# Kernel tuning notes

Measured on AMD Instinct MI355X. Metric: run time of the kernel, lower is better.

The kernel has to match this reference:

```python
import jax, jax.numpy as jnp
import numpy as np

D_MODEL = 1024
N_HEADS = 16
D_FF = 4096
B, T = 4, 2048
EPS = 1e-5


def layernorm(x, g, b):
    mu = jnp.mean(x, axis=-1, keepdims=True)
    var = jnp.var(x, axis=-1, keepdims=True)
    return (x - mu) * jax.lax.rsqrt(var + EPS) * g + b


def setup_inputs() -> dict:
    key = jax.random.key(0)
    ks = jax.random.split(key, 8)
    s = 0.02
    return {
        "x": jax.random.normal(ks[0], (B, T, D_MODEL), jnp.float32),
        "ln1_g": jnp.ones((D_MODEL,), jnp.float32),
        "ln1_b": jnp.zeros((D_MODEL,), jnp.float32),
        "wq": jax.random.normal(ks[1], (D_MODEL, D_MODEL), jnp.float32) * s,
        "bq": jnp.zeros((D_MODEL,), jnp.float32),
        "wk": jax.random.normal(ks[2], (D_MODEL, D_MODEL), jnp.float32) * s,
        "bk": jnp.zeros((D_MODEL,), jnp.float32),
        "wv": jax.random.normal(ks[3], (D_MODEL, D_MODEL), jnp.float32) * s,
        "bv": jnp.zeros((D_MODEL,), jnp.float32),
        "wo": jax.random.normal(ks[4], (D_MODEL, D_MODEL), jnp.float32) * s,
        "bo": jnp.zeros((D_MODEL,), jnp.float32),
        "ln2_g": jnp.ones((D_MODEL,), jnp.float32),
        "ln2_b": jnp.zeros((D_MODEL,), jnp.float32),
        "w1": jax.random.normal(ks[5], (D_FF, D_MODEL), jnp.float32) * s,
        "b1": jnp.zeros((D_FF,), jnp.float32),
        "w2": jax.random.normal(ks[6], (D_MODEL, D_FF), jnp.float32) * s,
        "b2": jnp.zeros((D_MODEL,), jnp.float32),
    }


def reference(x, ln1_g, ln1_b, wq, bq, wk, bk, wv, bv, wo, bo,
              ln2_g, ln2_b, w1, b1, w2, b2):
    d_k = D_MODEL // N_HEADS
    # --- attention sublayer (pre-LN) ---
    h = layernorm(x, ln1_g, ln1_b)                       # [B,T,D]
    q = (h @ wq.T + bq).reshape(B, T, N_HEADS, d_k)
    k = (h @ wk.T + bk).reshape(B, T, N_HEADS, d_k)
    v = (h @ wv.T + bv).reshape(B, T, N_HEADS, d_k)
    scores = jnp.einsum("bqhd,bkhd->bhqk", q, k) / jnp.sqrt(jnp.float32(d_k))
    attn = jax.nn.softmax(scores, axis=-1)               # [B,H,T,T]
    o = jnp.einsum("bhqk,bkhd->bqhd", attn, v).reshape(B, T, D_MODEL)
    x = x + (o @ wo.T + bo)
    # --- FFN sublayer ---
    h2 = layernorm(x, ln2_g, ln2_b)
    h2 = jax.nn.gelu(h2 @ w1.T + b1, approximate=False)  # torch GELU = exact erf
    x = x + (h2 @ w2.T + b2)
    return x
```

## Files before the change

kernel.cpp:

```cpp
#include <hip/hip_runtime.h>
#include <math.h>


#define D_MODEL 1024
#define D_FF    4096
#define NH      16
#define BATCH   4
#define SEQ     2048
#define DK      64
#define MTOK    (BATCH*SEQ)
#define NBH     (BATCH*NH)

typedef __bf16 bf16;
typedef _Float16 f16;
typedef bf16  bf16x4 __attribute__((ext_vector_type(4)));
typedef bf16  bf16x8 __attribute__((ext_vector_type(8)));
typedef f16   f16x4  __attribute__((ext_vector_type(4)));
typedef f16   f16x8  __attribute__((ext_vector_type(8)));
typedef __fp16 hf16x2 __attribute__((ext_vector_type(2)));
typedef __fp16 hf16x4 __attribute__((ext_vector_type(4)));
typedef __fp16 hf16x8 __attribute__((ext_vector_type(8)));
typedef float f32x4  __attribute__((ext_vector_type(4)));

__device__ __forceinline__ void gload_lds16(const void* g, void* l) {
  __builtin_amdgcn_global_load_lds(
      (__attribute__((address_space(1))) void*)g,
      (__attribute__((address_space(3))) void*)l, 16, 0, 0);
}

#define BAR() __builtin_amdgcn_s_barrier()
#define WAIT_VM0() do { asm volatile("s_waitcnt vmcnt(0)" ::: "memory"); \
  __builtin_amdgcn_sched_barrier(0); } while (0)

__device__ __forceinline__ float gelu_fast(float x) {
  float ax = fabsf(x) * 0.70710678118654752f;
  float t  = 1.0f / (1.0f + 0.3275911f * ax);
  float p  = t * (0.254829592f + t * (-0.284496736f + t * (1.421413741f +
             t * (-1.453152027f + t * 1.061405429f))));
  float e  = __builtin_amdgcn_exp2f(ax * ax * -1.4426950408889634f);
  float er = 1.0f - p * e;
  er = __builtin_copysignf(er, x);
  return 0.5f * x * (1.0f + er);
}

__global__ __launch_bounds__(256) void cast_w(const float* __restrict__ s,
                                              bf16* __restrict__ d, int n) {
  int i = (blockIdx.x * 256 + threadIdx.x) * 4;
  if (i >= n) return;
  float4 v = *(const float4*)(s + i);
  bf16x4 o;
  o[0] = (bf16)v.x; o[1] = (bf16)v.y; o[2] = (bf16)v.z; o[3] = (bf16)v.w;
  *(bf16x4*)(d + i) = o;
}

__global__ __launch_bounds__(256) void ln_kernel(const float* __restrict__ x,
                                                 const float* __restrict__ g,
                                                 const float* __restrict__ b,
                                                 bf16* __restrict__ out) {
  int row = blockIdx.x;
  int tid = threadIdx.x;
  const float* xr = x + (size_t)row * D_MODEL;
  float4 v = *(const float4*)(xr + tid * 4);
  float s  = v.x + v.y + v.z + v.w;
  float sq = v.x*v.x + v.y*v.y + v.z*v.z + v.w*v.w;
  #pragma unroll
  for (int off = 1; off < 64; off <<= 1) {
    s  += __shfl_xor(s,  off, 64);
    sq += __shfl_xor(sq, off, 64);
  }
  __shared__ float ls[4], lq[4];
  int wid = tid >> 6, lane = tid & 63;
  if (lane == 0) { ls[wid] = s; lq[wid] = sq; }
  __syncthreads();
  s  = ls[0] + ls[1] + ls[2] + ls[3];
  sq = lq[0] + lq[1] + lq[2] + lq[3];
  float mu   = s * (1.0f / D_MODEL);
  float var  = sq * (1.0f / D_MODEL) - mu * mu;
  float rstd = rsqrtf(var + 1e-5f);
  float4 gv = *(const float4*)(g + tid * 4);
  float4 bv = *(const float4*)(b + tid * 4);
  bf16x4 o;
  o[0] = (bf16)((v.x - mu) * rstd * gv.x + bv.x);
  o[1] = (bf16)((v.y - mu) * rstd * gv.y + bv.y);
  o[2] = (bf16)((v.z - mu) * rstd * gv.z + bv.z);
  o[3] = (bf16)((v.w - mu) * rstd * gv.w + bv.w);
  *(bf16x4*)(out + (size_t)row * D_MODEL + tid * 4) = o;
}

enum { EP_QKV = 0, EP_RESID = 1, EP_GELU = 2 };

#define QSCALE 0.18033688011112042f

template <int EP, int CFG>
__global__ __launch_bounds__(512) void gemm8p(
    const bf16* __restrict__ A, const bf16* __restrict__ W,
    const float* __restrict__ bias,
    const float* __restrict__ resid,
    float* __restrict__ out_f32,
    bf16* __restrict__ out_bf,
    int M, int N, int K) {
  constexpr int BM  = CFG ? 128 : 256;
  constexpr int BK  = CFG ? 64 : 32;
  constexpr int WM  = CFG ? 64 : 128;
  constexpr int FRN = WM / 16;
  constexpr int KKN = BK / 32;
  constexpr int RB  = BK * 2;
  constexpr int GR  = RB / 16;
  constexpr int RSH = CFG ? 7 : 6;
  constexpr int AB  = 16384;
  constexpr int TB  = AB + 256 * BK * 2;
  constexpr int L   = TB / 8192;

  __shared__ char lds[3 * TB];

  int tiles_n = N >> 8;
  int nwg = (M / BM) * tiles_n;
  int bid = blockIdx.x;
  int swz = (bid & 7) * (nwg >> 3) + (bid >> 3);
  int bm = swz / tiles_n, bn = swz % tiles_n;
  int m0 = bm * BM, n0 = bn << 8;
  int tid = threadIdx.x, wid = tid >> 6, lane = tid & 63;
  int wm = wid >> 2, wn = wid & 3;
  int l15 = lane & 15, l4 = lane >> 4;

  f32x4 acc[FRN][4];
  #pragma unroll
  for (int i = 0; i < FRN; i++)
    #pragma unroll
    for (int j = 0; j < 4; j++)
      #pragma unroll
      for (int e = 0; e < 4; e++) acc[i][j][e] = 0.f;

  auto STAGE = [&](int kt, int nb) {
    char* buf = lds + nb * TB;
    #pragma unroll
    for (int l = 0; l < L; ++l) {
      bool isA = l < 2;
      int o = (isA ? l : l - 2) * 8192 + tid * 16;
      int row = o >> RSH;
      int g = (o >> 4) & (GR - 1);
      int gs = g ^ (CFG ? (row & 7) : ((row >> 1) & 3));
      const bf16* src = (isA ? A + (size_t)(m0 + row) * K
                             : W + (size_t)(n0 + row) * K) + kt * BK + gs * 8;
      gload_lds16(src, buf + (isA ? 0 : AB) + o);
    }
  };

  int nt = K / BK;
  STAGE(0, 0);
  STAGE(1, 1);
  if constexpr (CFG) { asm volatile("s_waitcnt vmcnt(6)" ::: "memory"); }
  else               { asm volatile("s_waitcnt vmcnt(4)" ::: "memory"); }
  __builtin_amdgcn_sched_barrier(0);
  BAR();

  for (int t = 0; t < nt; ++t) {
    int cb = t % 3, nb = cb >= 1 ? cb - 1 : 2;
    const char* bc = lds + cb * TB;

    if (t + 2 < nt) STAGE(t + 2, nb);

    bf16x8 af[FRN][KKN], bfr[4][KKN];
    #pragma unroll
    for (int f = 0; f < FRN; ++f)
      #pragma unroll
      for (int kk = 0; kk < KKN; ++kk) {
        int row = wm * WM + f * 16 + l15;
        int g = (kk * 4 + l4) ^ (CFG ? (row & 7) : ((row >> 1) & 3));
        af[f][kk] = *(const bf16x8*)(bc + row * RB + g * 16);
      }
    #pragma unroll
    for (int fc = 0; fc < 4; ++fc)
      #pragma unroll
      for (int kk = 0; kk < KKN; ++kk) {
        int row = wn * 64 + fc * 16 + l15;
        int g = (kk * 4 + l4) ^ (CFG ? (row & 7) : ((row >> 1) & 3));
        bfr[fc][kk] = *(const bf16x8*)(bc + AB + row * RB + g * 16);
      }

    __builtin_amdgcn_s_setprio(1);
    #pragma unroll
    for (int f = 0; f < FRN; ++f)
      #pragma unroll
      for (int fc = 0; fc < 4; ++fc)
        #pragma unroll
        for (int kk = 0; kk < KKN; ++kk) {
          if (EP == EP_QKV)
            acc[f][fc] = __builtin_amdgcn_mfma_f32_16x16x32_bf16(af[f][kk], bfr[fc][kk],
                                                                 acc[f][fc], 0, 0, 0);
          else
            acc[f][fc] = __builtin_amdgcn_mfma_f32_16x16x32_bf16(bfr[fc][kk], af[f][kk],
                                                                 acc[f][fc], 0, 0, 0);
        }
    __builtin_amdgcn_s_setprio(0);

    if (t + 2 < nt) {
      if constexpr (CFG) { asm volatile("s_waitcnt vmcnt(6)" ::: "memory"); }
      else               { asm volatile("s_waitcnt vmcnt(4)" ::: "memory"); }
      __builtin_amdgcn_sched_barrier(0);
    } else if (t + 1 < nt) {
      WAIT_VM0();
    }
    BAR();
  }

  if (EP == EP_QKV) {
    #pragma unroll
    for (int i = 0; i < FRN; i++)
      #pragma unroll
      for (int j = 0; j < 4; j++) {
        int gm0 = m0 + wm * WM + i * 16 + (l4 << 2);
        int gn  = n0 + wn * 64 + j * 16 + l15;
        int which = gn >> 10;
        int nn = gn & 1023, head = nn >> 6, d = nn & 63;
        int bb = gm0 >> 11, t = gm0 & 2047;
        float bv = bias[gn];
        if (which == 2) {
          int sbase = (t & ~31) + ((t >> 2) & 3) * 8 + ((t >> 4) & 1) * 4;
          f16x4 pk;
          #pragma unroll
          for (int jj = 0; jj < 4; jj++) pk[jj] = (f16)(acc[i][j][jj] + bv);
          *(f16x4*)((f16*)out_bf + (size_t)2 * NBH * SEQ * DK +
                    ((size_t)(bb * NH + head) * DK + d) * SEQ + sbase) = pk;
        } else {
          float scale = (which == 0) ? QSCALE : 1.0f;
          #pragma unroll
          for (int jj = 0; jj < 4; jj++) {
            float cv = (acc[i][j][jj] + bv) * scale;
            size_t idx = (size_t)which * (NBH * SEQ * DK) +
                         ((size_t)(bb * NH + head) * SEQ + (t + jj)) * DK + d;
            out_bf[idx] = (bf16)cv;
          }
        }
      }
  } else {
    #pragma unroll
    for (int i = 0; i < FRN; i++) {
      int gm = m0 + wm * WM + i * 16 + l15;
      #pragma unroll
      for (int j = 0; j < 4; j++) {
        int gn = n0 + wn * 64 + j * 16 + (l4 << 2);
        float4 bv4 = *(const float4*)(bias + gn);
        size_t idx = (size_t)gm * N + gn;
        if (EP == EP_RESID) {
          float4 rv = *(const float4*)(resid + idx);
          float4 ov;
          ov.x = rv.x + acc[i][j][0] + bv4.x;
          ov.y = rv.y + acc[i][j][1] + bv4.y;
          ov.z = rv.z + acc[i][j][2] + bv4.z;
          ov.w = rv.w + acc[i][j][3] + bv4.w;
          *(float4*)(out_f32 + idx) = ov;
        } else {
          bf16x4 pk;
          pk[0] = (bf16)gelu_fast(acc[i][j][0] + bv4.x);
          pk[1] = (bf16)gelu_fast(acc[i][j][1] + bv4.y);
          pk[2] = (bf16)gelu_fast(acc[i][j][2] + bv4.z);
          pk[3] = (bf16)gelu_fast(acc[i][j][3] + bv4.w);
          *(bf16x4*)(out_bf + idx) = pk;
        }
      }
    }
  }
}

__global__ __launch_bounds__(512) void attn_kernel(
    const bf16* __restrict__ q, const bf16* __restrict__ k,
    const f16* __restrict__ vt, bf16* __restrict__ o) {
  __shared__ bf16 kt_lds[2][64 * 64];
  __shared__ f16  vt_lds[2][64 * 64];
  int bid = blockIdx.x;
  int swzb = (bid & 7) * 64 + (bid >> 3);
  int bh = swzb >> 3;
  int qt = swzb & 7;
  int t0 = qt << 8;
  int tid = threadIdx.x, wid = tid >> 6, lane = tid & 63;
  int l15 = lane & 15, l4 = lane >> 4;

  int kb0 = l15 * 128 + ((l4 ^ (l15 & 7)) << 4);
  int kb1 = l15 * 128 + (((4 + l4) ^ (l15 & 7)) << 4);
  int vb32[2];
  #pragma unroll
  for (int n = 0; n < 2; n++)
    vb32[n] = l15 * 128 + (((n * 4 + l4) ^ (l15 & 7)) << 4);

  bf16x8 qf[2][2];
  #pragma unroll
  for (int qr = 0; qr < 2; qr++) {
    const bf16* qbase = q + ((size_t)bh * SEQ + t0 + wid * 32 + qr * 16 + l15) * DK;
    qf[qr][0] = *(const bf16x8*)(qbase + (l4 << 3));
    qf[qr][1] = *(const bf16x8*)(qbase + 32 + (l4 << 3));
  }

  f16x8 vones8;
  #pragma unroll
  for (int e = 0; e < 8; e++) vones8[e] = (f16)1.f;
  float m_run[2] = {-1e30f, -1e30f};
  f32x4 acc_o[2][4];
  f32x4 acc_l[2];
  #pragma unroll
  for (int qr = 0; qr < 2; qr++) {
    #pragma unroll
    for (int nd = 0; nd < 4; nd++)
      #pragma unroll
      for (int e = 0; e < 4; e++) acc_o[qr][nd][e] = 0.f;
    #pragma unroll
    for (int e = 0; e < 4; e++) acc_l[qr][e] = 0.f;
  }

  int oK = tid * 16;
  int rowk = oK >> 7, gk = (oK >> 4) & 7;
  const bf16* gKsrc = k + ((size_t)bh * SEQ + rowk) * DK + ((gk ^ (rowk & 7)) << 3);
  int dV = oK >> 7, gd = (oK >> 4) & 7;
  const f16* gVsrc = vt + ((size_t)bh * DK + dV) * SEQ + ((gd ^ (dV & 7)) << 3);

  auto stage = [&](int buf, int t) {
    int kv0 = t * 64;
    gload_lds16(gKsrc + (size_t)kv0 * DK, (char*)&kt_lds[buf][0] + tid * 16);
    gload_lds16(gVsrc + kv0, (char*)&vt_lds[buf][0] + tid * 16);
  };

  stage(0, 0);
  WAIT_VM0();
  BAR();

  for (int t = 0; t < SEQ / 64; ++t) {
    int cur = t & 1;
    if (t < SEQ / 64 - 1) stage(cur ^ 1, t + 1);
    const char* kbase = (const char*)&kt_lds[cur][0];
    const char* vbase = (const char*)&vt_lds[cur][0];

    f32x4 accs[2][4];
    #pragma unroll
    for (int qr = 0; qr < 2; qr++)
      #pragma unroll
      for (int n = 0; n < 4; n++)
        #pragma unroll
        for (int e = 0; e < 4; e++) accs[qr][n][e] = 0.f;
    __builtin_amdgcn_s_setprio(1);
    #pragma unroll
    for (int n = 0; n < 4; n++) {
      bf16x8 kf0 = *(const bf16x8*)(kbase + kb0 + n * 2048);
      bf16x8 kf1 = *(const bf16x8*)(kbase + kb1 + n * 2048);
      #pragma unroll
      for (int qr = 0; qr < 2; qr++) {
        accs[qr][n] = __builtin_amdgcn_mfma_f32_16x16x32_bf16(kf0, qf[qr][0], accs[qr][n], 0, 0, 0);
        accs[qr][n] = __builtin_amdgcn_mfma_f32_16x16x32_bf16(kf1, qf[qr][1], accs[qr][n], 0, 0, 0);
      }
    }
    __builtin_amdgcn_s_setprio(0);

    f16x8 pa32[2][2];
    #pragma unroll
    for (int qr = 0; qr < 2; qr++) {
      float mloc = -1e30f;
      #pragma unroll
      for (int n = 0; n < 4; n++) {
        float a0 = fmaxf(accs[qr][n][0], accs[qr][n][1]);
        float a1 = fmaxf(accs[qr][n][2], accs[qr][n][3]);
        mloc = fmaxf(mloc, fmaxf(a0, a1));
      }
      float mt = fmaxf(mloc, __shfl_xor(mloc, 16, 64));
      mt = fmaxf(mt, __shfl_xor(mt, 32, 64));
      if (__any(mt > m_run[qr] + 8.0f)) {
        float mn = fmaxf(m_run[qr], mt);
        float sc = __builtin_amdgcn_exp2f(m_run[qr] - mn);
        m_run[qr] = mn;
        float scr0 = __shfl(sc, l4 * 20 + 0, 64);
        float scr1 = __shfl(sc, l4 * 20 + 1, 64);
        float scr2 = __shfl(sc, l4 * 20 + 2, 64);
        float scr3 = __shfl(sc, l4 * 20 + 3, 64);
        #pragma unroll
        for (int nd = 0; nd < 4; nd++) {
          acc_o[qr][nd][0] *= scr0; acc_o[qr][nd][1] *= scr1;
          acc_o[qr][nd][2] *= scr2; acc_o[qr][nd][3] *= scr3;
        }
        acc_l[qr][0] *= scr0; acc_l[qr][1] *= scr1;
        acc_l[qr][2] *= scr2; acc_l[qr][3] *= scr3;
      }
      #pragma unroll
      for (int n = 0; n < 2; n++) {
        float e0 = __builtin_amdgcn_exp2f(accs[qr][2*n][0] - m_run[qr]);
        float e1 = __builtin_amdgcn_exp2f(accs[qr][2*n][1] - m_run[qr]);
        float e2 = __builtin_amdgcn_exp2f(accs[qr][2*n][2] - m_run[qr]);
        float e3 = __builtin_amdgcn_exp2f(accs[qr][2*n][3] - m_run[qr]);
        float e4 = __builtin_amdgcn_exp2f(accs[qr][2*n+1][0] - m_run[qr]);
        float e5 = __builtin_amdgcn_exp2f(accs[qr][2*n+1][1] - m_run[qr]);
        float e6 = __builtin_amdgcn_exp2f(accs[qr][2*n+1][2] - m_run[qr]);
        float e7 = __builtin_amdgcn_exp2f(accs[qr][2*n+1][3] - m_run[qr]);
        hf16x2 p01 = __builtin_amdgcn_cvt_pkrtz(e0, e1);
        hf16x2 p23 = __builtin_amdgcn_cvt_pkrtz(e2, e3);
        hf16x2 p45 = __builtin_amdgcn_cvt_pkrtz(e4, e5);
        hf16x2 p67 = __builtin_amdgcn_cvt_pkrtz(e6, e7);
        hf16x4 lo = __builtin_shufflevector(p01, p23, 0, 1, 2, 3);
        hf16x4 hi = __builtin_shufflevector(p45, p67, 0, 1, 2, 3);
        hf16x8 cmb = __builtin_shufflevector(lo, hi, 0, 1, 2, 3, 4, 5, 6, 7);
        pa32[qr][n] = __builtin_bit_cast(f16x8, cmb);
      }
    }

    __builtin_amdgcn_s_setprio(1);
    #pragma unroll
    for (int n = 0; n < 2; n++) {
      #pragma unroll
      for (int nd = 0; nd < 4; nd++) {
        f16x8 vf = *(const f16x8*)(vbase + vb32[n] + nd * 2048);
        #pragma unroll
        for (int qr = 0; qr < 2; qr++)
          acc_o[qr][nd] = __builtin_amdgcn_mfma_f32_16x16x32_f16(pa32[qr][n], vf, acc_o[qr][nd], 0, 0, 0);
      }
      #pragma unroll
      for (int qr = 0; qr < 2; qr++)
        acc_l[qr] = __builtin_amdgcn_mfma_f32_16x16x32_f16(pa32[qr][n], vones8, acc_l[qr], 0, 0, 0);
    }
    __builtin_amdgcn_s_setprio(0);

    if (t < SEQ / 64 - 1) { WAIT_VM0(); }
    BAR();
  }

  int bb = bh >> 4, hh = bh & 15;
  #pragma unroll
  for (int qr = 0; qr < 2; qr++) {
    float rl0 = 1.0f / acc_l[qr][0], rl1 = 1.0f / acc_l[qr][1];
    float rl2 = 1.0f / acc_l[qr][2], rl3 = 1.0f / acc_l[qr][3];
    int rowb = t0 + wid * 32 + qr * 16 + l4 * 4;
    #pragma unroll
    for (int nd = 0; nd < 4; nd++) {
      int d = nd * 16 + l15;
      o[((size_t)bb * SEQ + rowb + 0) * D_MODEL + hh * DK + d] = (bf16)(acc_o[qr][nd][0] * rl0);
      o[((size_t)bb * SEQ + rowb + 1) * D_MODEL + hh * DK + d] = (bf16)(acc_o[qr][nd][1] * rl1);
      o[((size_t)bb * SEQ + rowb + 2) * D_MODEL + hh * DK + d] = (bf16)(acc_o[qr][nd][2] * rl2);
      o[((size_t)bb * SEQ + rowb + 3) * D_MODEL + hh * DK + d] = (bf16)(acc_o[qr][nd][3] * rl3);
    }
  }
}

extern "C" void kernel_launch(void* const* d_in, const int* in_sizes, int n_in,
                              void* d_out, int out_size, void* d_ws, size_t ws_size,
                              hipStream_t stream) {
  const float* x    = (const float*)d_in[0];
  const float* ln1g = (const float*)d_in[1];
  const float* ln1b = (const float*)d_in[2];
  const float* wq   = (const float*)d_in[3];
  const float* bq   = (const float*)d_in[4];
  const float* wk   = (const float*)d_in[5];
  const float* bk   = (const float*)d_in[6];
  const float* wv   = (const float*)d_in[7];
  const float* bv   = (const float*)d_in[8];
  const float* wo   = (const float*)d_in[9];
  const float* bo   = (const float*)d_in[10];
  const float* ln2g = (const float*)d_in[11];
  const float* ln2b = (const float*)d_in[12];
  const float* w1   = (const float*)d_in[13];
  const float* b1   = (const float*)d_in[14];
  const float* w2   = (const float*)d_in[15];
  const float* b2   = (const float*)d_in[16];
  float* out = (float*)d_out;

  char* ws = (char*)d_ws;
  bf16* wqkv_b = (bf16*)(ws);
  bf16* wo_b   = (bf16*)(ws + ((size_t)6  << 20));
  bf16* w1_b   = (bf16*)(ws + ((size_t)8  << 20));
  bf16* w2_b   = (bf16*)(ws + ((size_t)16 << 20));
  bf16* h_b    = (bf16*)(ws + ((size_t)24 << 20));
  bf16* qkv_b  = (bf16*)(ws + ((size_t)40 << 20));
  bf16* o_b    = (bf16*)(ws + ((size_t)88 << 20));
  bf16* ffn1_b = (bf16*)(ws + ((size_t)40 << 20));
  float* bqkv  = (float*)(ws + ((size_t)104 << 20));

  cast_w<<<1024, 256, 0, stream>>>(wq, wqkv_b, 1 << 20);
  cast_w<<<1024, 256, 0, stream>>>(wk, wqkv_b + (1 << 20), 1 << 20);
  cast_w<<<1024, 256, 0, stream>>>(wv, wqkv_b + (2 << 20), 1 << 20);
  cast_w<<<1024, 256, 0, stream>>>(wo, wo_b, 1 << 20);
  cast_w<<<4096, 256, 0, stream>>>(w1, w1_b, 1 << 22);
  cast_w<<<4096, 256, 0, stream>>>(w2, w2_b, 1 << 22);
  (void)hipMemcpyAsync(bqkv,        bq, 4096, hipMemcpyDeviceToDevice, stream);
  (void)hipMemcpyAsync(bqkv + 1024, bk, 4096, hipMemcpyDeviceToDevice, stream);
  (void)hipMemcpyAsync(bqkv + 2048, bv, 4096, hipMemcpyDeviceToDevice, stream);

  ln_kernel<<<MTOK, 256, 0, stream>>>(x, ln1g, ln1b, h_b);
  gemm8p<EP_QKV, 1><<<768, 512, 0, stream>>>(h_b, wqkv_b, bqkv, nullptr, nullptr,
                                             qkv_b, MTOK, 3072, 1024);
  attn_kernel<<<512, 512, 0, stream>>>(qkv_b, qkv_b + (size_t)NBH * SEQ * DK,
                                       (const f16*)(qkv_b + (size_t)2 * NBH * SEQ * DK),
                                       o_b);
  gemm8p<EP_RESID, 1><<<256, 512, 0, stream>>>(o_b, wo_b, bo, x, out, nullptr,
                                               MTOK, 1024, 1024);
  ln_kernel<<<MTOK, 256, 0, stream>>>(out, ln2g, ln2b, h_b);
  gemm8p<EP_GELU, 0><<<512, 512, 0, stream>>>(h_b, w1_b, b1, nullptr, nullptr,
                                              ffn1_b, MTOK, 4096, 1024);
  gemm8p<EP_RESID, 1><<<256, 512, 0, stream>>>(ffn1_b, w2_b, b2, out, out, nullptr,
                                               MTOK, 1024, 4096);
}
```

Baseline: 408.5 us.

## Use 256x256 GEMM tiles with quarter-staged double buffering for QKV and FFN1

Adds a new gemm256 kernel with 256x256 output tiles and BK=64, double-buffered in 128KB of LDS. Each k-step is split into four phases, one per B column fragment, and the next tile's loads are issued in quarter chunks between those phases. The QKV projection moves from 128x256 to 256x256 tiles, and FFN1 moves from BK=32 to 64, to raise data reuse per tile. The residual GEMMs get their own specialized kernel that keeps the old 128x256 configuration. In exchange there are many extra barriers per k-step, a large LDS footprint that limits occupancy, and fewer workgroups for QKV (384).

```diff
diff --git a/kernel.cpp b/kernel.cpp
--- a/kernel.cpp
+++ b/kernel.cpp
@@ -29,7 +29,11 @@
 }
 
 #define BAR() __builtin_amdgcn_s_barrier()
+#define LGKM0() do { asm volatile("s_waitcnt lgkmcnt(0)" ::: "memory"); \
+  __builtin_amdgcn_sched_barrier(0); } while (0)
 #define WAIT_VM0() do { asm volatile("s_waitcnt vmcnt(0)" ::: "memory"); \
+  __builtin_amdgcn_sched_barrier(0); } while (0)
+#define WAIT_VM4() do { asm volatile("s_waitcnt vmcnt(4)" ::: "memory"); \
   __builtin_amdgcn_sched_barrier(0); } while (0)
 
 __device__ __forceinline__ float gelu_fast(float x) {
@@ -88,128 +92,145 @@
 }
 
 enum { EP_QKV = 0, EP_RESID = 1, EP_GELU = 2 };
-
 #define QSCALE 0.18033688011112042f
 
-template <int EP, int CFG>
-__global__ __launch_bounds__(512) void gemm8p(
+template <int EP>
+__global__ __launch_bounds__(512, 2) void gemm256(
     const bf16* __restrict__ A, const bf16* __restrict__ W,
     const float* __restrict__ bias,
-    const float* __restrict__ resid,
-    float* __restrict__ out_f32,
     bf16* __restrict__ out_bf,
     int M, int N, int K) {
-  constexpr int BM  = CFG ? 128 : 256;
-  constexpr int BK  = CFG ? 64 : 32;
-  constexpr int WM  = CFG ? 64 : 128;
-  constexpr int FRN = WM / 16;
-  constexpr int KKN = BK / 32;
-  constexpr int RB  = BK * 2;
-  constexpr int GR  = RB / 16;
-  constexpr int RSH = CFG ? 7 : 6;
-  constexpr int AB  = 16384;
-  constexpr int TB  = AB + 256 * BK * 2;
-  constexpr int L   = TB / 8192;
-
-  __shared__ char lds[3 * TB];
-
+  __shared__ char lds[131072];
   int tiles_n = N >> 8;
-  int nwg = (M / BM) * tiles_n;
+  int nwg = (M >> 8) * tiles_n;
   int bid = blockIdx.x;
   int swz = (bid & 7) * (nwg >> 3) + (bid >> 3);
   int bm = swz / tiles_n, bn = swz % tiles_n;
-  int m0 = bm * BM, n0 = bn << 8;
+  int m0 = bm << 8, n0 = bn << 8;
   int tid = threadIdx.x, wid = tid >> 6, lane = tid & 63;
   int wm = wid >> 2, wn = wid & 3;
   int l15 = lane & 15, l4 = lane >> 4;
 
-  f32x4 acc[FRN][4];
-  #pragma unroll
-  for (int i = 0; i < FRN; i++)
-    #pragma unroll
-    for (int j = 0; j < 4; j++)
-      #pragma unroll
-      for (int e = 0; e < 4; e++) acc[i][j][e] = 0.f;
-
-  auto STAGE = [&](int kt, int nb) {
-    char* buf = lds + nb * TB;
-    #pragma unroll
-    for (int l = 0; l < L; ++l) {
-      bool isA = l < 2;
-      int o = (isA ? l : l - 2) * 8192 + tid * 16;
-      int row = o >> RSH;
-      int g = (o >> 4) & (GR - 1);
-      int gs = g ^ (CFG ? (row & 7) : ((row >> 1) & 3));
-      const bf16* src = (isA ? A + (size_t)(m0 + row) * K
-                             : W + (size_t)(n0 + row) * K) + kt * BK + gs * 8;
-      gload_lds16(src, buf + (isA ? 0 : AB) + o);
+  f32x4 acc[8][4];
+  #pragma unroll
+  for (int f = 0; f < 8; f++)
+    #pragma unroll
+    for (int n = 0; n < 4; n++)
+      #pragma unroll
+      for (int e = 0; e < 4; e++) acc[f][n][e] = 0.f;
+
+  auto STAGEH = [&](int h, int kt, int bsel) {
+    char* buf = lds + bsel * 65536;
+    #pragma unroll
+    for (int l = 0; l < 2; ++l) {
+      int o = h * 16384 + l * 8192 + tid * 16;
+      int row = (o >> 7) & 255;
+      int g = (o >> 4) & 7;
+      int gs = g ^ (row & 7);
+      const bf16* src = (h < 2 ? A + (size_t)(m0 + row) * K
+                               : W + (size_t)(n0 + row) * K) + kt * 64 + gs * 8;
+      gload_lds16(src, buf + o);
     }
   };
-
-  int nt = K / BK;
-  STAGE(0, 0);
-  STAGE(1, 1);
-  if constexpr (CFG) { asm volatile("s_waitcnt vmcnt(6)" ::: "memory"); }
-  else               { asm volatile("s_waitcnt vmcnt(4)" ::: "memory"); }
-  __builtin_amdgcn_sched_barrier(0);
+  auto RDB = [&](const char* bc, int n, int kk) -> bf16x8 {
+    int row = wn * 64 + n * 16 + l15;
+    return *(const bf16x8*)(bc + 32768 + row * 128 + (((kk << 2) + l4) ^ (row & 7)) * 16);
+  };
+
+  int nt = K >> 6;
+  STAGEH(0, 0, 0); STAGEH(1, 0, 0); STAGEH(2, 0, 0); STAGEH(3, 0, 0);
+  STAGEH(0, 1, 1); STAGEH(1, 1, 1);
+  WAIT_VM4();
   BAR();
 
   for (int t = 0; t < nt; ++t) {
-    int cb = t % 3, nb = cb >= 1 ? cb - 1 : 2;
-    const char* bc = lds + cb * TB;
-
-    if (t + 2 < nt) STAGE(t + 2, nb);
-
-    bf16x8 af[FRN][KKN], bfr[4][KKN];
-    #pragma unroll
-    for (int f = 0; f < FRN; ++f)
-      #pragma unroll
-      for (int kk = 0; kk < KKN; ++kk) {
-        int row = wm * WM + f * 16 + l15;
-        int g = (kk * 4 + l4) ^ (CFG ? (row & 7) : ((row >> 1) & 3));
-        af[f][kk] = *(const bf16x8*)(bc + row * RB + g * 16);
-      }
-    #pragma unroll
-    for (int fc = 0; fc < 4; ++fc)
-      #pragma unroll
-      for (int kk = 0; kk < KKN; ++kk) {
-        int row = wn * 64 + fc * 16 + l15;
-        int g = (kk * 4 + l4) ^ (CFG ? (row & 7) : ((row >> 1) & 3));
-        bfr[fc][kk] = *(const bf16x8*)(bc + AB + row * RB + g * 16);
-      }
-
+    const char* bc = lds + (t & 1) * 65536;
+    bf16x8 af[8][2];
+
+    #pragma unroll
+    for (int f = 0; f < 8; ++f)
+      #pragma unroll
+      for (int kk = 0; kk < 2; ++kk) {
+        int row = wm * 128 + f * 16 + l15;
+        af[f][kk] = *(const bf16x8*)(bc + row * 128 + (((kk << 2) + l4) ^ (row & 7)) * 16);
+      }
+    bf16x8 b0[2];
+    b0[0] = RDB(bc, 0, 0); b0[1] = RDB(bc, 0, 1);
+    if (t + 1 < nt) STAGEH(2, t + 1, (t + 1) & 1);
+    BAR(); LGKM0();
     __builtin_amdgcn_s_setprio(1);
     #pragma unroll
-    for (int f = 0; f < FRN; ++f)
-      #pragma unroll
-      for (int fc = 0; fc < 4; ++fc)
-        #pragma unroll
-        for (int kk = 0; kk < KKN; ++kk) {
-          if (EP == EP_QKV)
-            acc[f][fc] = __builtin_amdgcn_mfma_f32_16x16x32_bf16(af[f][kk], bfr[fc][kk],
-                                                                 acc[f][fc], 0, 0, 0);
-          else
-            acc[f][fc] = __builtin_amdgcn_mfma_f32_16x16x32_bf16(bfr[fc][kk], af[f][kk],
-                                                                 acc[f][fc], 0, 0, 0);
-        }
+    for (int f = 0; f < 8; ++f)
+      #pragma unroll
+      for (int kk = 0; kk < 2; ++kk) {
+        if (EP == EP_QKV)
+          acc[f][0] = __builtin_amdgcn_mfma_f32_16x16x32_bf16(af[f][kk], b0[kk], acc[f][0], 0, 0, 0);
+        else
+          acc[f][0] = __builtin_amdgcn_mfma_f32_16x16x32_bf16(b0[kk], af[f][kk], acc[f][0], 0, 0, 0);
+      }
     __builtin_amdgcn_s_setprio(0);
-
-    if (t + 2 < nt) {
-      if constexpr (CFG) { asm volatile("s_waitcnt vmcnt(6)" ::: "memory"); }
-      else               { asm volatile("s_waitcnt vmcnt(4)" ::: "memory"); }
-      __builtin_amdgcn_sched_barrier(0);
-    } else if (t + 1 < nt) {
-      WAIT_VM0();
-    }
     BAR();
+
+    bf16x8 b1[2];
+    b1[0] = RDB(bc, 1, 0); b1[1] = RDB(bc, 1, 1);
+    if (t + 1 < nt) STAGEH(3, t + 1, (t + 1) & 1);
+    BAR(); LGKM0();
+    __builtin_amdgcn_s_setprio(1);
+    #pragma unroll
+    for (int f = 0; f < 8; ++f)
+      #pragma unroll
+      for (int kk = 0; kk < 2; ++kk) {
+        if (EP == EP_QKV)
+          acc[f][1] = __builtin_amdgcn_mfma_f32_16x16x32_bf16(af[f][kk], b1[kk], acc[f][1], 0, 0, 0);
+        else
+          acc[f][1] = __builtin_amdgcn_mfma_f32_16x16x32_bf16(b1[kk], af[f][kk], acc[f][1], 0, 0, 0);
+      }
+    __builtin_amdgcn_s_setprio(0);
+    BAR();
+
+    bf16x8 b2[2];
+    b2[0] = RDB(bc, 2, 0); b2[1] = RDB(bc, 2, 1);
+    if (t + 2 < nt) STAGEH(0, t + 2, t & 1);
+    BAR(); LGKM0();
+    __builtin_amdgcn_s_setprio(1);
+    #pragma unroll
+    for (int f = 0; f < 8; ++f)
+      #pragma unroll
+      for (int kk = 0; kk < 2; ++kk) {
+        if (EP == EP_QKV)
+          acc[f][2] = __builtin_amdgcn_mfma_f32_16x16x32_bf16(af[f][kk], b2[kk], acc[f][2], 0, 0, 0);
+        else
+          acc[f][2] = __builtin_amdgcn_mfma_f32_16x16x32_bf16(b2[kk], af[f][kk], acc[f][2], 0, 0, 0);
+      }
+    __builtin_amdgcn_s_setprio(0);
+    BAR();
+
+    bf16x8 b3[2];
+    b3[0] = RDB(bc, 3, 0); b3[1] = RDB(bc, 3, 1);
+    if (t + 2 < nt) STAGEH(1, t + 2, t & 1);
+    BAR(); LGKM0();
+    __builtin_amdgcn_s_setprio(1);
+    #pragma unroll
+    for (int f = 0; f < 8; ++f)
+      #pragma unroll
+      for (int kk = 0; kk < 2; ++kk) {
+        if (EP == EP_QKV)
+          acc[f][3] = __builtin_amdgcn_mfma_f32_16x16x32_bf16(af[f][kk], b3[kk], acc[f][3], 0, 0, 0);
+        else
+          acc[f][3] = __builtin_amdgcn_mfma_f32_16x16x32_bf16(b3[kk], af[f][kk], acc[f][3], 0, 0, 0);
+      }
+    __builtin_amdgcn_s_setprio(0);
+    if (t + 2 < nt)      { WAIT_VM4(); }
+    else if (t + 1 < nt) { WAIT_VM0(); }
+    BAR();
   }
 
   if (EP == EP_QKV) {
     #pragma unroll
-    for (int i = 0; i < FRN; i++)
+    for (int i = 0; i < 8; i++)
       #pragma unroll
       for (int j = 0; j < 4; j++) {
-        int gm0 = m0 + wm * WM + i * 16 + (l4 << 2);
+        int gm0 = m0 + wm * 128 + i * 16 + (l4 << 2);
         int gn  = n0 + wn * 64 + j * 16 + l15;
         int which = gn >> 10;
         int nn = gn & 1023, head = nn >> 6, d = nn & 63;
@@ -235,30 +256,129 @@
       }
   } else {
     #pragma unroll
-    for (int i = 0; i < FRN; i++) {
-      int gm = m0 + wm * WM + i * 16 + l15;
+    for (int i = 0; i < 8; i++) {
+      int gm = m0 + wm * 128 + i * 16 + l15;
       #pragma unroll
       for (int j = 0; j < 4; j++) {
         int gn = n0 + wn * 64 + j * 16 + (l4 << 2);
         float4 bv4 = *(const float4*)(bias + gn);
-        size_t idx = (size_t)gm * N + gn;
-        if (EP == EP_RESID) {
-          float4 rv = *(const float4*)(resid + idx);
-          float4 ov;
-          ov.x = rv.x + acc[i][j][0] + bv4.x;
-          ov.y = rv.y + acc[i][j][1] + bv4.y;
-          ov.z = rv.z + acc[i][j][2] + bv4.z;
-          ov.w = rv.w + acc[i][j][3] + bv4.w;
-          *(float4*)(out_f32 + idx) = ov;
-        } else {
-          bf16x4 pk;
-          pk[0] = (bf16)gelu_fast(acc[i][j][0] + bv4.x);
-          pk[1] = (bf16)gelu_fast(acc[i][j][1] + bv4.y);
-          pk[2] = (bf16)gelu_fast(acc[i][j][2] + bv4.z);
-          pk[3] = (bf16)gelu_fast(acc[i][j][3] + bv4.w);
-          *(bf16x4*)(out_bf + idx) = pk;
-        }
-      }
+        bf16x4 pk;
+        pk[0] = (bf16)gelu_fast(acc[i][j][0] + bv4.x);
+        pk[1] = (bf16)gelu_fast(acc[i][j][1] + bv4.y);
+        pk[2] = (bf16)gelu_fast(acc[i][j][2] + bv4.z);
+        pk[3] = (bf16)gelu_fast(acc[i][j][3] + bv4.w);
+        *(bf16x4*)(out_bf + (size_t)gm * N + gn) = pk;
+      }
+    }
+  }
+}
+
+__global__ __launch_bounds__(512) void gemm_resid(
+    const bf16* __restrict__ A, const bf16* __restrict__ W,
+    const float* __restrict__ bias,
+    const float* __restrict__ resid,
+    float* __restrict__ out_f32,
+    int M, int N, int K) {
+  constexpr int BK = 64, RB = 128;
+  constexpr int AB = 16384, TB = 49152, L = 6;
+  __shared__ char lds[3 * TB];
+
+  int tiles_n = N >> 8;
+  int nwg = (M >> 7) * tiles_n;
+  int bid = blockIdx.x;
+  int swz = (bid & 7) * (nwg >> 3) + (bid >> 3);
+  int bm = swz / tiles_n, bn = swz % tiles_n;
+  int m0 = bm << 7, n0 = bn << 8;
+  int tid = threadIdx.x, wid = tid >> 6, lane = tid & 63;
+  int wm = wid >> 2, wn = wid & 3;
+  int l15 = lane & 15, l4 = lane >> 4;
+
+  f32x4 acc[4][4];
+  #pragma unroll
+  for (int i = 0; i < 4; i++)
+    #pragma unroll
+    for (int j = 0; j < 4; j++)
+      #pragma unroll
+      for (int e = 0; e < 4; e++) acc[i][j][e] = 0.f;
+
+  auto STAGE = [&](int kt, int nb) {
+    char* buf = lds + nb * TB;
+    #pragma unroll
+    for (int l = 0; l < L; ++l) {
+      bool isA = l < 2;
+      int o = (isA ? l : l - 2) * 8192 + tid * 16;
+      int row = o >> 7;
+      int g = (o >> 4) & 7;
+      int gs = g ^ (row & 7);
+      const bf16* src = (isA ? A + (size_t)(m0 + row) * K
+                             : W + (size_t)(n0 + row) * K) + kt * BK + gs * 8;
+      gload_lds16(src, buf + (isA ? 0 : AB) + o);
+    }
+  };
+
+  int nt = K / BK;
+  STAGE(0, 0);
+  STAGE(1, 1);
+  asm volatile("s_waitcnt vmcnt(6)" ::: "memory");
+  __builtin_amdgcn_sched_barrier(0);
+  BAR();
+
+  for (int t = 0; t < nt; ++t) {
+    int cb = t % 3, nb = cb >= 1 ? cb - 1 : 2;
+    const char* bc = lds + cb * TB;
+    if (t + 2 < nt) STAGE(t + 2, nb);
+
+    bf16x8 af[4][2], bfr[4][2];
+    #pragma unroll
+    for (int f = 0; f < 4; ++f)
+      #pragma unroll
+      for (int kk = 0; kk < 2; ++kk) {
+        int row = wm * 64 + f * 16 + l15;
+        af[f][kk] = *(const bf16x8*)(bc + row * RB + (((kk << 2) + l4) ^ (row & 7)) * 16);
+      }
+    #pragma unroll
+    for (int fc = 0; fc < 4; ++fc)
+      #pragma unroll
+      for (int kk = 0; kk < 2; ++kk) {
+        int row = wn * 64 + fc * 16 + l15;
+        bfr[fc][kk] = *(const bf16x8*)(bc + AB + row * RB + (((kk << 2) + l4) ^ (row & 7)) * 16);
+      }
+
+    __builtin_amdgcn_s_setprio(1);
+    #pragma unroll
+    for (int f = 0; f < 4; ++f)
+      #pragma unroll
+      for (int fc = 0; fc < 4; ++fc)
+        #pragma unroll
+        for (int kk = 0; kk < 2; ++kk)
+          acc[f][fc] = __builtin_amdgcn_mfma_f32_16x16x32_bf16(bfr[fc][kk], af[f][kk],
+                                                               acc[f][fc], 0, 0, 0);
+    __builtin_amdgcn_s_setprio(0);
+
+    if (t + 2 < nt) {
+      asm volatile("s_waitcnt vmcnt(6)" ::: "memory");
+      __builtin_amdgcn_sched_barrier(0);
+    } else if (t + 1 < nt) {
+      WAIT_VM0();
+    }
+    BAR();
+  }
+
+  #pragma unroll
+  for (int i = 0; i < 4; i++) {
+    int gm = m0 + wm * 64 + i * 16 + l15;
+    #pragma unroll
+    for (int j = 0; j < 4; j++) {
+      int gn = n0 + wn * 64 + j * 16 + (l4 << 2);
+      float4 bv4 = *(const float4*)(bias + gn);
+      size_t idx = (size_t)gm * N + gn;
+      float4 rv = *(const float4*)(resid + idx);
+      float4 ov;
+      ov.x = rv.x + acc[i][j][0] + bv4.x;
+      ov.y = rv.y + acc[i][j][1] + bv4.y;
+      ov.z = rv.z + acc[i][j][2] + bv4.z;
+      ov.w = rv.w + acc[i][j][3] + bv4.w;
+      *(float4*)(out_f32 + idx) = ov;
     }
   }
 }
@@ -479,16 +599,14 @@
   (void)hipMemcpyAsync(bqkv + 2048, bv, 4096, hipMemcpyDeviceToDevice, stream);
 
   ln_kernel<<<MTOK, 256, 0, stream>>>(x, ln1g, ln1b, h_b);
-  gemm8p<EP_QKV, 1><<<768, 512, 0, stream>>>(h_b, wqkv_b, bqkv, nullptr, nullptr,
-                                             qkv_b, MTOK, 3072, 1024);
+  gemm256<EP_QKV><<<384, 512, 0, stream>>>(h_b, wqkv_b, bqkv, qkv_b,
+                                           MTOK, 3072, 1024);
   attn_kernel<<<512, 512, 0, stream>>>(qkv_b, qkv_b + (size_t)NBH * SEQ * DK,
                                        (const f16*)(qkv_b + (size_t)2 * NBH * SEQ * DK),
                                        o_b);
-  gemm8p<EP_RESID, 1><<<256, 512, 0, stream>>>(o_b, wo_b, bo, x, out, nullptr,
-                                               MTOK, 1024, 1024);
+  gemm_resid<<<256, 512, 0, stream>>>(o_b, wo_b, bo, x, out, MTOK, 1024, 1024);
   ln_kernel<<<MTOK, 256, 0, stream>>>(out, ln2g, ln2b, h_b);
-  gemm8p<EP_GELU, 0><<<512, 512, 0, stream>>>(h_b, w1_b, b1, nullptr, nullptr,
-                                              ffn1_b, MTOK, 4096, 1024);
-  gemm8p<EP_RESID, 1><<<256, 512, 0, stream>>>(ffn1_b, w2_b, b2, out, out, nullptr,
-                                               MTOK, 1024, 4096);
-}
+  gemm256<EP_GELU><<<512, 512, 0, stream>>>(h_b, w1_b, b1, ffn1_b,
+                                            MTOK, 4096, 1024);
+  gemm_resid<<<256, 512, 0, stream>>>(ffn1_b, w2_b, b2, out, out, MTOK, 1024, 4096);
+}
```

Result: faster. 392.8 us (-3.8%).
